# Optimization experiments

Hardware: AMD Instinct MI355X
Metric: run time of the kernel (lower is better)

Reference implementation:

```python
import jax, jax.numpy as jnp
import numpy as np

D_MODEL = 1024
H = 16
T = 1024
B = 8

def setup_inputs() -> dict:
    key = jax.random.key(0)
    k0, k1, k2, k3, k4 = jax.random.split(key, 5)
    return {
        "x": jax.random.normal(k0, (B, T, D_MODEL), dtype=jnp.float32),
        "Wq": jax.random.normal(k1, (D_MODEL, D_MODEL), dtype=jnp.float32),
        "Wk": jax.random.normal(k2, (D_MODEL, D_MODEL), dtype=jnp.float32),
        "Wv": jax.random.normal(k3, (D_MODEL, D_MODEL), dtype=jnp.float32),
        "Wp": jax.random.normal(k4, (D_MODEL, D_MODEL), dtype=jnp.float32),
    }

def reference(x, Wq, Wk, Wv, Wp):
    b, t, d = x.shape
    dh = d // H
    # projections
    q = (x @ Wq).reshape(b, t, H, dh)
    k = (x @ Wk).reshape(b, t, H, dh)
    v = (x @ Wv).reshape(b, t, H, dh)
    # [b, h, t, t] attention scores, scaled by sqrt(d_head)
    scores = jnp.einsum("bqhd,bkhd->bhqk", q, k) / jnp.sqrt(jnp.float32(dh))
    attn = jax.nn.softmax(scores, axis=-1)
    # [b, h, t, dh] -> [b, t, d]
    out = jnp.einsum("bhqk,bkhd->bqhd", attn, v).reshape(b, t, d)
    return out @ Wp
```

## Files before the change

kernel.cpp:

```cpp
#include <hip/hip_runtime.h>
#include <math.h>


typedef unsigned short u16;
typedef unsigned int u32;
typedef __bf16  bf16x8 __attribute__((ext_vector_type(8)));
typedef unsigned short u16x8 __attribute__((ext_vector_type(8)));
typedef unsigned short u16x4 __attribute__((ext_vector_type(4)));
typedef short s16x4 __attribute__((ext_vector_type(4)));
typedef unsigned int u32x2 __attribute__((ext_vector_type(2)));
typedef float f32x4 __attribute__((ext_vector_type(4)));

#define MFMA16(a,b,c) __builtin_amdgcn_mfma_f32_16x16x32_bf16((a),(b),(c),0,0,0)
#define MFMA16K16(a,b,c) __builtin_amdgcn_mfma_f32_16x16x16bf16_1k((a),(b),(c),0,0,0)

static __device__ __forceinline__ u16 f2b(float f){
  unsigned u = __builtin_bit_cast(unsigned, f);
  u += 0x7fffu + ((u >> 16) & 1u);
  return (u16)(u >> 16);
}
static __device__ __forceinline__ float b2f(u16 h){
  unsigned u = ((unsigned)h) << 16;
  return __builtin_bit_cast(float, u);
}
static __device__ __forceinline__ bf16x8 ldsfrag(const u16* p){
  return __builtin_bit_cast(bf16x8, *(const u16x8*)p);
}
static __device__ __forceinline__ u32 packhi(float fa, float fb){
  return __builtin_amdgcn_perm(__builtin_bit_cast(u32, fa),
                               __builtin_bit_cast(u32, fb), 0x07060302u);
}
static __device__ __forceinline__ void gld16(const void* g, void* l){
  __builtin_amdgcn_global_load_lds(
      (const __attribute__((address_space(1))) void*)g,
      (__attribute__((address_space(3))) void*)l, 16, 0, 0);
}


__global__ __launch_bounds__(256) void split_x_kernel(
    const float* __restrict__ x, u16* __restrict__ xh, u16* __restrict__ xl, int n)
{
  int i = (blockIdx.x * 256 + threadIdx.x) * 8;
  if (i >= n) return;
  float4 v0 = *(const float4*)(x + i);
  float4 v1 = *(const float4*)(x + i + 4);
  float vv[8] = {v0.x, v0.y, v0.z, v0.w, v1.x, v1.y, v1.z, v1.w};
  u16x8 hv, lv;
#pragma unroll
  for (int j = 0; j < 8; j++){
    u16 hb = f2b(vv[j]);
    hv[j] = hb;
    lv[j] = f2b(vv[j] - b2f(hb));
  }
  *(u16x8*)(xh + i) = hv;
  *(u16x8*)(xl + i) = lv;
}

__global__ __launch_bounds__(256) void transpose4_kernel(
    const float* __restrict__ Wq, const float* __restrict__ Wk,
    const float* __restrict__ Wv, const float* __restrict__ Wp,
    u16* __restrict__ qh_, u16* __restrict__ ql_,
    u16* __restrict__ kh_, u16* __restrict__ kl_,
    u16* __restrict__ vt_, u16* __restrict__ pt_)
{
  __shared__ float t[32][33];
  const int z = blockIdx.z;
  const float* W = (z == 0) ? Wq : (z == 1) ? Wk : (z == 2) ? Wv : Wp;
  u16* Th = (z == 0) ? qh_ : (z == 1) ? kh_ : (z == 2) ? vt_ : pt_;
  u16* Tl = (z == 0) ? ql_ : (z == 1) ? kl_ : nullptr;
  int n0 = blockIdx.x * 32, k0 = blockIdx.y * 32;
  int tx = threadIdx.x, ty = threadIdx.y;
#pragma unroll
  for (int i = 0; i < 4; i++){
    int k = k0 + ty + i * 8;
    t[ty + i * 8][tx] = W[(size_t)k * 1024 + n0 + tx];
  }
  __syncthreads();
#pragma unroll
  for (int i = 0; i < 4; i++){
    int n = n0 + ty + i * 8;
    float v = t[tx][ty + i * 8];
    u16 h = f2b(v);
    Th[(size_t)n * 1024 + k0 + tx] = h;
    if (Tl) Tl[(size_t)n * 1024 + k0 + tx] = f2b(v - b2f(h));
  }
}

template<int OUTMODE>
__global__ __launch_bounds__(256) void gemm_bt_kernel(
    const u16* __restrict__ A, const u16* __restrict__ Bt, void* __restrict__ Cv,
    int M, int N, int K)
{
  __shared__ __attribute__((aligned(16))) u16 lA[4096], lB[4096];
  const int tid = threadIdx.x, lane = tid & 63, wave = tid >> 6;
  const int quad = lane >> 4, l15 = lane & 15;
  const int row0 = blockIdx.x * 128, col0 = blockIdx.y * 128;
  const int wm = wave >> 1, wn = wave & 1;
  const int sr = lane >> 2, sc = (lane & 3) * 8;
  f32x4 acc[4][4];
#pragma unroll
  for (int mt = 0; mt < 4; mt++)
#pragma unroll
    for (int nt = 0; nt < 4; nt++) acc[mt][nt] = (f32x4)0.0f;

  for (int k0 = 0; k0 < K; k0 += 32){
#pragma unroll
    for (int i = 0; i < 2; i++){
      int c = wave * 2 + i;
      gld16(A  + (size_t)(row0 + c * 16 + sr) * K + k0 + sc, &lA[c * 512]);
      gld16(Bt + (size_t)(col0 + c * 16 + sr) * K + k0 + sc, &lB[c * 512]);
    }
    __syncthreads();
    bf16x8 a[4], b[4];
#pragma unroll
    for (int t = 0; t < 4; t++){
      a[t] = ldsfrag(&lA[(wm * 64 + t * 16 + l15) * 32 + quad * 8]);
      b[t] = ldsfrag(&lB[(wn * 64 + t * 16 + l15) * 32 + quad * 8]);
    }
#pragma unroll
    for (int mt = 0; mt < 4; mt++)
#pragma unroll
      for (int nt = 0; nt < 4; nt++)
        acc[mt][nt] = MFMA16(a[mt], b[nt], acc[mt][nt]);
    __syncthreads();
  }
  if (OUTMODE == 2){
#pragma unroll
    for (int mt = 0; mt < 4; mt++)
#pragma unroll
      for (int nt = 0; nt < 4; nt++){
        int row = row0 + wm * 64 + mt * 16 + quad * 4;
        int col = col0 + wn * 64 + nt * 16 + l15;
        int bb = row >> 10, tt = row & 1023;
        int hh = (col >> 6) & 15, d = col & 63;
        int bhI = bb * 16 + hh;
        int ktile = tt >> 7, fkt = (tt >> 4) & 7, qF = (tt >> 2) & 3;
        int nd = d >> 4, l15F = d & 15;
        size_t idx = ((((size_t)(bhI * 8 + ktile) * 8 + fkt) * 4 + nd) * 64
                      + qF * 16 + l15F) * 4;
        u16x4 vals;
#pragma unroll
        for (int r = 0; r < 4; r++) vals[r] = f2b(acc[mt][nt][r]);
        *(u16x4*)(((u16*)Cv) + idx) = vals;
      }
  } else {
#pragma unroll
    for (int mt = 0; mt < 4; mt++)
#pragma unroll
      for (int nt = 0; nt < 4; nt++)
#pragma unroll
        for (int r = 0; r < 4; r++){
          int row = row0 + wm * 64 + mt * 16 + quad * 4 + r;
          int col = col0 + wn * 64 + nt * 16 + l15;
          ((float*)Cv)[(size_t)row * N + col] = acc[mt][nt][r];
        }
  }
}

__global__ __launch_bounds__(512, 2) void gemm_qk_kernel(
    const u16* __restrict__ Ah, const u16* __restrict__ Al,
    const u16* __restrict__ Bh, const u16* __restrict__ Bl,
    u16* __restrict__ Qhf, u16* __restrict__ Qlf,
    u16* __restrict__ Khf, u16* __restrict__ Klf, int M, int N, int K)
{
  __shared__ __attribute__((aligned(16))) u16 sA[2][2][8192], sB[2][2][8192];
  const int tid = threadIdx.x, lane = tid & 63, wave = tid >> 6;
  const int quad = lane >> 4, l15 = lane & 15;
  const int wm = wave >> 2, wn = wave & 3;
  const int row0 = blockIdx.x * 256, col0 = blockIdx.y * 256;
  const int f0a = (wave & 3) | ((wave & 4) << 1);
  const int f0b = (wave & 1) | ((wave >> 1) << 2);
  const size_t fstride = (size_t)16 * K;
  const size_t abase = (size_t)(row0 + l15) * K + quad * 8;
  const size_t bbase = (size_t)(col0 + l15) * K + quad * 8;
  (void)M; (void)N;

  f32x4 acc[8][4];
#pragma unroll
  for (int mt = 0; mt < 8; mt++)
#pragma unroll
    for (int nt = 0; nt < 4; nt++) acc[mt][nt] = (f32x4)0.0f;

#define STAGE_G0(KK, NB) do {                                              \
    gld16(Ah + abase + (size_t)f0a * fstride + (KK), &sA[NB][0][f0a * 512]); \
    gld16(Al + abase + (size_t)f0a * fstride + (KK), &sA[NB][1][f0a * 512]); \
    gld16(Bh + bbase + (size_t)f0b * fstride + (KK), &sB[NB][0][f0b * 512]); \
    gld16(Bl + bbase + (size_t)f0b * fstride + (KK), &sB[NB][1][f0b * 512]); \
  } while (0)
#define STAGE_G1(KK, NB) do {                                                        \
    gld16(Bh + bbase + (size_t)(f0b + 2) * fstride + (KK), &sB[NB][0][(f0b + 2) * 512]); \
    gld16(Bl + bbase + (size_t)(f0b + 2) * fstride + (KK), &sB[NB][1][(f0b + 2) * 512]); \
  } while (0)
#define STAGE_G2(KK, NB) do {                                                        \
    gld16(Ah + abase + (size_t)(f0a + 4) * fstride + (KK), &sA[NB][0][(f0a + 4) * 512]); \
    gld16(Al + abase + (size_t)(f0a + 4) * fstride + (KK), &sA[NB][1][(f0a + 4) * 512]); \
  } while (0)
#define RD_A(B4, BUF) do {                                        \
    _Pragma("unroll")                                             \
    for (int i = 0; i < 4; i++){                                  \
      int fa = wm * 8 + (B4) + i;                                 \
      ahf[i] = ldsfrag(&sA[BUF][0][fa * 512 + lane * 8]);         \
      alf[i] = ldsfrag(&sA[BUF][1][fa * 512 + lane * 8]);         \
    } } while (0)
#define RD_B(B2, BUF) do {                                        \
    _Pragma("unroll")                                             \
    for (int j = 0; j < 2; j++){                                  \
      int fb = wn * 4 + (B2) + j;                                 \
      bhf[j] = ldsfrag(&sB[BUF][0][fb * 512 + lane * 8]);         \
      blf[j] = ldsfrag(&sB[BUF][1][fb * 512 + lane * 8]);         \
    } } while (0)
#define MM(M0, N0) do {                                                      \
    __builtin_amdgcn_s_setprio(1);                                           \
    _Pragma("unroll")                                                        \
    for (int i = 0; i < 4; i++)                                              \
      _Pragma("unroll")                                                      \
      for (int j = 0; j < 2; j++){                                           \
        acc[(M0) + i][(N0) + j] = MFMA16(alf[i], bhf[j], acc[(M0) + i][(N0) + j]); \
        acc[(M0) + i][(N0) + j] = MFMA16(ahf[i], blf[j], acc[(M0) + i][(N0) + j]); \
        acc[(M0) + i][(N0) + j] = MFMA16(ahf[i], bhf[j], acc[(M0) + i][(N0) + j]); \
      }                                                                      \
    __builtin_amdgcn_s_setprio(0);                                           \
  } while (0)
#define VMCNT4() asm volatile("s_waitcnt vmcnt(4)" ::: "memory")
#define VMCNT6() asm volatile("s_waitcnt vmcnt(6)" ::: "memory")
#define BARRIER() asm volatile("s_barrier" ::: "memory")

  const int NT = K >> 5;
  STAGE_G0(0, 0);
  STAGE_G1(0, 0);
  STAGE_G2(0, 0);

  bf16x8 ahf[4], alf[4], bhf[2], blf[2];
#pragma unroll 2
  for (int t = 0; t < NT; t++){
    const int buf = t & 1, nb = buf ^ 1;
    const int kn = ((t + 1) & (NT - 1)) * 32;
    VMCNT4();
    BARRIER();
    RD_A(0, buf);
    RD_B(0, buf);
    STAGE_G0(kn, nb);
    MM(0, 0);
    VMCNT6();
    BARRIER();
    RD_B(2, buf);
    STAGE_G1(kn, nb);
    MM(0, 2);
    VMCNT6();
    BARRIER();
    RD_A(4, buf);
    STAGE_G2(kn, nb);
    MM(4, 2);
    RD_B(0, buf);
    MM(4, 0);
  }
  asm volatile("s_waitcnt vmcnt(0)" ::: "memory");

#undef STAGE_G0
#undef STAGE_G1
#undef STAGE_G2
#undef RD_A
#undef RD_B
#undef MM
#undef VMCNT4
#undef VMCNT6
#undef BARRIER

  const bool isQ = (col0 < 1024);
#pragma unroll
  for (int mt = 0; mt < 8; mt++)
#pragma unroll
    for (int nt = 0; nt < 4; nt++)
#pragma unroll
      for (int r = 0; r < 4; r++){
        int row = row0 + wm * 128 + mt * 16 + quad * 4 + r;
        int col = col0 + wn * 64 + nt * 16 + l15;
        int bb = row >> 10, tt = row & 1023;
        int hh = (col >> 6) & 15, d = col & 63;
        int bhI = bb * 16 + hh;
        int kc = d >> 5, qF = (d >> 3) & 3, j = d & 7;
        float v = acc[mt][nt][r];
        u16 hi = f2b(v);
        u16 lo = f2b(v - b2f(hi));
        if (isQ){
          int qtile = tt >> 7, rr = tt & 127;
          int wv = rr >> 5, mtF = (rr >> 4) & 1, l15F = tt & 15;
          size_t idx = ((((size_t)(bhI * 8 + qtile) * 4 + wv) * 2 + mtF) * 2 + kc) * 512
                       + (qF * 16 + l15F) * 8 + j;
          Qhf[idx] = hi; Qlf[idx] = lo;
        } else {
          int ktile = tt >> 7, fkt = (tt >> 4) & 7, l15F = tt & 15;
          size_t idx = (((size_t)(bhI * 8 + ktile) * 8 + fkt) * 2 + kc) * 512
                       + (qF * 16 + l15F) * 8 + j;
          Khf[idx] = hi; Klf[idx] = lo;
        }
      }
}

__global__ __launch_bounds__(256, 3) void attn_kernel(
    const u16* __restrict__ Qhf, const u16* __restrict__ Qlf,
    const u16* __restrict__ Khf, const u16* __restrict__ Klf,
    const u16* __restrict__ Vf, u16* __restrict__ O)
{
  __shared__ __attribute__((aligned(16))) u16 lKh[2][4096], lKl[2][4096], lV[2][4096];
  const int tid = threadIdx.x, lane = tid & 63, wave = tid >> 6;
  const int quad = lane >> 4, l15 = lane & 15;
  const int qt = blockIdx.x >> 7, bh = blockIdx.x & 127;
  const int b = bh >> 4, h = bh & 15;
  const int q0 = qt * 128;
  const float BETA = 0.18033688011112042f;

  bf16x8 qh[2][2], ql[2][2];
  {
    size_t qbase = (size_t)(bh * 8 + qt) * 8192 + wave * 2048 + lane * 8;
    u16* sh = &lKh[0][0];  u16* sl = &lKl[0][0];
#pragma unroll
    for (int i = 0; i < 4; i++){
      gld16(Qhf + qbase + i * 512, sh + wave * 2048 + i * 512);
      gld16(Qlf + qbase + i * 512, sl + wave * 2048 + i * 512);
    }
    __syncthreads();
#pragma unroll
    for (int mt = 0; mt < 2; mt++)
#pragma unroll
      for (int kc = 0; kc < 2; kc++){
        int off = wave * 2048 + (mt * 2 + kc) * 512 + lane * 8;
        qh[mt][kc] = ldsfrag(sh + off);
        ql[mt][kc] = ldsfrag(sl + off);
      }
    __syncthreads();
  }

  float m_i[2] = {-3.0e38f, -3.0e38f}, l_i[2] = {0.0f, 0.0f};
  f32x4 o_acc[2][4];
#pragma unroll
  for (int mt = 0; mt < 2; mt++)
#pragma unroll
    for (int nd = 0; nd < 4; nd++) o_acc[mt][nd] = (f32x4)0.0f;

  const size_t pan = (size_t)bh * 65536;
#pragma unroll
  for (int i = 0; i < 2; i++){
    int c = wave * 2 + i;
    gld16(Khf + pan + c * 512 + lane * 8, &lKh[0][c * 512]);
    gld16(Klf + pan + c * 512 + lane * 8, &lKl[0][c * 512]);
    gld16(Vf  + pan + c * 512 + lane * 8, &lV [0][c * 512]);
  }

#pragma unroll 1
  for (int j = 0; j < 16; j++){
    const int cur = j & 1;
    __syncthreads();
    if (j < 15){
      size_t nb = pan + (size_t)(j + 1) * 4096;
      const int nxt = cur ^ 1;
#pragma unroll
      for (int i = 0; i < 2; i++){
        int c = wave * 2 + i;
        gld16(Khf + nb + c * 512 + lane * 8, &lKh[nxt][c * 512]);
        gld16(Klf + nb + c * 512 + lane * 8, &lKl[nxt][c * 512]);
        gld16(Vf  + nb + c * 512 + lane * 8, &lV [nxt][c * 512]);
      }
    }

    f32x4 s[2][4];
#pragma unroll
    for (int qt2 = 0; qt2 < 2; qt2++)
#pragma unroll
      for (int f4 = 0; f4 < 4; f4++) s[qt2][f4] = (f32x4)0.0f;
#pragma unroll
    for (int f4 = 0; f4 < 4; f4++){
      int aoff = f4 * 1024 + lane * 8;
      bf16x8 kh0 = ldsfrag(&lKh[cur][aoff]);
      bf16x8 kh1 = ldsfrag(&lKh[cur][aoff + 512]);
      bf16x8 kl0 = ldsfrag(&lKl[cur][aoff]);
      bf16x8 kl1 = ldsfrag(&lKl[cur][aoff + 512]);
      __builtin_amdgcn_s_setprio(1);
#pragma unroll
      for (int qt2 = 0; qt2 < 2; qt2++){
        s[qt2][f4] = MFMA16(kl0, qh[qt2][0], s[qt2][f4]);
        s[qt2][f4] = MFMA16(kl1, qh[qt2][1], s[qt2][f4]);
        s[qt2][f4] = MFMA16(kh0, ql[qt2][0], s[qt2][f4]);
        s[qt2][f4] = MFMA16(kh1, ql[qt2][1], s[qt2][f4]);
        s[qt2][f4] = MFMA16(kh0, qh[qt2][0], s[qt2][f4]);
        s[qt2][f4] = MFMA16(kh1, qh[qt2][1], s[qt2][f4]);
      }
      __builtin_amdgcn_s_setprio(0);
    }

    float alpha[2];
#pragma unroll
    for (int qt2 = 0; qt2 < 2; qt2++){
      f32x4 mv = s[qt2][0];
#pragma unroll
      for (int f4 = 1; f4 < 4; f4++){
        mv[0] = fmaxf(mv[0], s[qt2][f4][0]); mv[1] = fmaxf(mv[1], s[qt2][f4][1]);
        mv[2] = fmaxf(mv[2], s[qt2][f4][2]); mv[3] = fmaxf(mv[3], s[qt2][f4][3]);
      }
      float mx = fmaxf(fmaxf(mv[0], mv[1]), fmaxf(mv[2], mv[3]));
      mx = fmaxf(mx, __shfl_xor(mx, 16));
      mx = fmaxf(mx, __shfl_xor(mx, 32));
      float mn = fmaxf(m_i[qt2], mx);
      alpha[qt2] = __builtin_amdgcn_exp2f((m_i[qt2] - mn) * BETA);
      m_i[qt2] = mn;
      float mb = mn * BETA;
      f32x4 ps = (f32x4)0.0f;
#pragma unroll
      for (int f4 = 0; f4 < 4; f4++)
#pragma unroll
        for (int r = 0; r < 4; r++){
          float p = __builtin_amdgcn_exp2f(s[qt2][f4][r] * BETA - mb);
          s[qt2][f4][r] = p;
          ps[r] += p;
        }
      float rs = (ps[0] + ps[1]) + (ps[2] + ps[3]);
      rs += __shfl_xor(rs, 16);
      rs += __shfl_xor(rs, 32);
      l_i[qt2] = l_i[qt2] * alpha[qt2] + rs;
    }

#pragma unroll
    for (int mt = 0; mt < 2; mt++)
#pragma unroll
      for (int r = 0; r < 4; r++){
        float ar = __shfl(alpha[mt], quad * 4 + r);
#pragma unroll
        for (int nd = 0; nd < 4; nd++) o_acc[mt][nd][r] *= ar;
      }

#pragma unroll
    for (int f4 = 0; f4 < 4; f4++){
      s16x4 vb[4];
#pragma unroll
      for (int nd = 0; nd < 4; nd++)
        vb[nd] = __builtin_bit_cast(s16x4,
                   *(const u16x4*)&lV[cur][(f4 * 4 + nd) * 256 + lane * 4]);
      __builtin_amdgcn_s_setprio(1);
#pragma unroll
      for (int qt2 = 0; qt2 < 2; qt2++){
        u32x2 pd;
        pd[0] = packhi(s[qt2][f4][1], s[qt2][f4][0]);
        pd[1] = packhi(s[qt2][f4][3], s[qt2][f4][2]);
        s16x4 pa = __builtin_bit_cast(s16x4, pd);
#pragma unroll
        for (int nd = 0; nd < 4; nd++)
          o_acc[qt2][nd] = MFMA16K16(pa, vb[nd], o_acc[qt2][nd]);
      }
      __builtin_amdgcn_s_setprio(0);
    }
  }

#pragma unroll
  for (int mt = 0; mt < 2; mt++)
#pragma unroll
    for (int r = 0; r < 4; r++){
      float lr = __shfl(l_i[mt], quad * 4 + r);
      float inv = 1.0f / lr;
      int t = q0 + wave * 32 + mt * 16 + quad * 4 + r;
      size_t rowoff = (size_t)(b * 1024 + t) * 1024 + h * 64;
#pragma unroll
      for (int nd = 0; nd < 4; nd++)
        O[rowoff + nd * 16 + l15] = f2b(o_acc[mt][nd][r] * inv);
    }
}

extern "C" void kernel_launch(void* const* d_in, const int* in_sizes, int n_in,
                              void* d_out, int out_size, void* d_ws, size_t ws_size,
                              hipStream_t stream)
{
  const float* x  = (const float*)d_in[0];
  const float* Wq = (const float*)d_in[1];
  const float* Wk = (const float*)d_in[2];
  const float* Wv = (const float*)d_in[3];
  const float* Wp = (const float*)d_in[4];
  float* out = (float*)d_out;
  char* ws = (char*)d_ws;
  const size_t MB = 1024 * 1024;
  u16* xh   = (u16*)(ws + 0);
  u16* xl   = (u16*)(ws + 16 * MB);
  u16* wqkh = (u16*)(ws + 32 * MB);
  u16* wqkl = (u16*)(ws + 36 * MB);
  u16* wvt  = (u16*)(ws + 40 * MB);
  u16* wpt  = (u16*)(ws + 42 * MB);
  u16* Qhf  = (u16*)(ws + 44 * MB);
  u16* Qlf  = (u16*)(ws + 60 * MB);
  u16* Khf  = (u16*)(ws + 76 * MB);
  u16* Klf  = (u16*)(ws + 92 * MB);
  u16* Vf   = (u16*)(ws + 108 * MB);
  u16* obuf = xh;
  (void)in_sizes; (void)n_in; (void)out_size; (void)ws_size;

  split_x_kernel<<<4096, 256, 0, stream>>>(x, xh, xl, 8 * 1024 * 1024);
  transpose4_kernel<<<dim3(32, 32, 4), dim3(32, 8), 0, stream>>>(
      Wq, Wk, Wv, Wp, wqkh, wqkl, wqkh + 1024 * 1024, wqkl + 1024 * 1024, wvt, wpt);
  gemm_qk_kernel<<<dim3(32, 8), 512, 0, stream>>>(xh, xl, wqkh, wqkl,
                                                  Qhf, Qlf, Khf, Klf, 8192, 2048, 1024);
  gemm_bt_kernel<2><<<dim3(64, 8), 256, 0, stream>>>(xh, wvt, (void*)Vf, 8192, 1024, 1024);
  attn_kernel<<<1024, 256, 0, stream>>>(Qhf, Qlf, Khf, Klf, Vf, obuf);
  gemm_bt_kernel<0><<<dim3(64, 8), 256, 0, stream>>>(obuf, wpt, (void*)out, 8192, 1024, 1024);
}
```

Baseline: 335.0 us.

## Double-buffer LDS tiles in bf16 GEMM with one barrier per k-step

```diff
diff --git a/kernel.cpp b/kernel.cpp
--- a/kernel.cpp
+++ b/kernel.cpp
@@ -91,39 +91,54 @@
     const u16* __restrict__ A, const u16* __restrict__ Bt, void* __restrict__ Cv,
     int M, int N, int K)
 {
-  __shared__ __attribute__((aligned(16))) u16 lA[4096], lB[4096];
+  __shared__ __attribute__((aligned(16))) u16 lA[2][4096], lB[2][4096];
   const int tid = threadIdx.x, lane = tid & 63, wave = tid >> 6;
   const int quad = lane >> 4, l15 = lane & 15;
   const int row0 = blockIdx.x * 128, col0 = blockIdx.y * 128;
   const int wm = wave >> 1, wn = wave & 1;
-  const int sr = lane >> 2, sc = (lane & 3) * 8;
+  const int c0 = wave * 2, c1 = wave * 2 + 1;
+  const size_t ar0 = (size_t)(row0 + c0 * 16 + l15) * K + quad * 8;
+  const size_t ar1 = (size_t)(row0 + c1 * 16 + l15) * K + quad * 8;
+  const size_t br0 = (size_t)(col0 + c0 * 16 + l15) * K + quad * 8;
+  const size_t br1 = (size_t)(col0 + c1 * 16 + l15) * K + quad * 8;
   f32x4 acc[4][4];
 #pragma unroll
   for (int mt = 0; mt < 4; mt++)
 #pragma unroll
     for (int nt = 0; nt < 4; nt++) acc[mt][nt] = (f32x4)0.0f;
 
-  for (int k0 = 0; k0 < K; k0 += 32){
-#pragma unroll
-    for (int i = 0; i < 2; i++){
-      int c = wave * 2 + i;
-      gld16(A  + (size_t)(row0 + c * 16 + sr) * K + k0 + sc, &lA[c * 512]);
-      gld16(Bt + (size_t)(col0 + c * 16 + sr) * K + k0 + sc, &lB[c * 512]);
-    }
-    __syncthreads();
+  const int NT = K >> 5;
+  gld16(A  + ar0, &lA[0][c0 * 512]);
+  gld16(A  + ar1, &lA[0][c1 * 512]);
+  gld16(Bt + br0, &lB[0][c0 * 512]);
+  gld16(Bt + br1, &lB[0][c1 * 512]);
+
+#pragma unroll 2
+  for (int t = 0; t < NT; t++){
+    const int buf = t & 1, nb = buf ^ 1;
+    const int kn = ((t + 1) & (NT - 1)) * 32;
+    asm volatile("s_waitcnt vmcnt(0)" ::: "memory");
+    asm volatile("s_barrier" ::: "memory");
+    gld16(A  + ar0 + kn, &lA[nb][c0 * 512]);
+    gld16(A  + ar1 + kn, &lA[nb][c1 * 512]);
+    gld16(Bt + br0 + kn, &lB[nb][c0 * 512]);
+    gld16(Bt + br1 + kn, &lB[nb][c1 * 512]);
     bf16x8 a[4], b[4];
 #pragma unroll
-    for (int t = 0; t < 4; t++){
-      a[t] = ldsfrag(&lA[(wm * 64 + t * 16 + l15) * 32 + quad * 8]);
-      b[t] = ldsfrag(&lB[(wn * 64 + t * 16 + l15) * 32 + quad * 8]);
-    }
+    for (int f = 0; f < 4; f++){
+      a[f] = ldsfrag(&lA[buf][(wm * 4 + f) * 512 + lane * 8]);
+      b[f] = ldsfrag(&lB[buf][(wn * 4 + f) * 512 + lane * 8]);
+    }
+    __builtin_amdgcn_s_setprio(1);
 #pragma unroll
     for (int mt = 0; mt < 4; mt++)
 #pragma unroll
       for (int nt = 0; nt < 4; nt++)
         acc[mt][nt] = MFMA16(a[mt], b[nt], acc[mt][nt]);
-    __syncthreads();
-  }
+    __builtin_amdgcn_s_setprio(0);
+  }
+  asm volatile("s_waitcnt vmcnt(0)" ::: "memory");
+
   if (OUTMODE == 2){
 #pragma unroll
     for (int mt = 0; mt < 4; mt++)
```

After: 356.0 us. 6.3% more time.

## Process two query tiles per attention block to reuse K/V panels

Applied to the files above, without the earlier changes.

```diff
diff --git a/kernel.cpp b/kernel.cpp
--- a/kernel.cpp
+++ b/kernel.cpp
@@ -297,7 +297,7 @@
       }
 }
 
-__global__ __launch_bounds__(256, 3) void attn_kernel(
+__global__ __launch_bounds__(256, 2) void attn_kernel(
     const u16* __restrict__ Qhf, const u16* __restrict__ Qlf,
     const u16* __restrict__ Khf, const u16* __restrict__ Klf,
     const u16* __restrict__ Vf, u16* __restrict__ O)
@@ -307,36 +307,42 @@
   const int quad = lane >> 4, l15 = lane & 15;
   const int qt = blockIdx.x >> 7, bh = blockIdx.x & 127;
   const int b = bh >> 4, h = bh & 15;
-  const int q0 = qt * 128;
+  const int q0 = qt * 256;
   const float BETA = 0.18033688011112042f;
 
-  bf16x8 qh[2][2], ql[2][2];
+  bf16x8 qh[2][2][2], ql[2][2][2];
   {
-    size_t qbase = (size_t)(bh * 8 + qt) * 8192 + wave * 2048 + lane * 8;
     u16* sh = &lKh[0][0];  u16* sl = &lKl[0][0];
 #pragma unroll
-    for (int i = 0; i < 4; i++){
-      gld16(Qhf + qbase + i * 512, sh + wave * 2048 + i * 512);
-      gld16(Qlf + qbase + i * 512, sl + wave * 2048 + i * 512);
+    for (int g = 0; g < 2; g++){
+      size_t qbase = ((size_t)((bh * 8 + 2 * qt + g) * 4 + wave)) * 2048 + lane * 8;
+#pragma unroll
+      for (int i = 0; i < 4; i++){
+        gld16(Qhf + qbase + i * 512, sh + wave * 2048 + i * 512);
+        gld16(Qlf + qbase + i * 512, sl + wave * 2048 + i * 512);
+      }
+      __syncthreads();
+#pragma unroll
+      for (int mt = 0; mt < 2; mt++)
+#pragma unroll
+        for (int kc = 0; kc < 2; kc++){
+          int off = wave * 2048 + (mt * 2 + kc) * 512 + lane * 8;
+          qh[g][mt][kc] = ldsfrag(sh + off);
+          ql[g][mt][kc] = ldsfrag(sl + off);
+        }
+      __syncthreads();
     }
-    __syncthreads();
+  }
+
+  float m_i[2][2] = {{-3.0e38f, -3.0e38f}, {-3.0e38f, -3.0e38f}};
+  float l_i[2][2] = {{0.0f, 0.0f}, {0.0f, 0.0f}};
+  f32x4 o_acc[2][2][4];
+#pragma unroll
+  for (int g = 0; g < 2; g++)
 #pragma unroll
     for (int mt = 0; mt < 2; mt++)
 #pragma unroll
-      for (int kc = 0; kc < 2; kc++){
-        int off = wave * 2048 + (mt * 2 + kc) * 512 + lane * 8;
-        qh[mt][kc] = ldsfrag(sh + off);
-        ql[mt][kc] = ldsfrag(sl + off);
-      }
-    __syncthreads();
-  }
-
-  float m_i[2] = {-3.0e38f, -3.0e38f}, l_i[2] = {0.0f, 0.0f};
-  f32x4 o_acc[2][4];
-#pragma unroll
-  for (int mt = 0; mt < 2; mt++)
-#pragma unroll
-    for (int nd = 0; nd < 4; nd++) o_acc[mt][nd] = (f32x4)0.0f;
+      for (int nd = 0; nd < 4; nd++) o_acc[g][mt][nd] = (f32x4)0.0f;
 
   const size_t pan = (size_t)bh * 65536;
 #pragma unroll
@@ -363,105 +369,110 @@
       }
     }
 
-    f32x4 s[2][4];
-#pragma unroll
-    for (int qt2 = 0; qt2 < 2; qt2++)
-#pragma unroll
-      for (int f4 = 0; f4 < 4; f4++) s[qt2][f4] = (f32x4)0.0f;
-#pragma unroll
-    for (int f4 = 0; f4 < 4; f4++){
-      int aoff = f4 * 1024 + lane * 8;
-      bf16x8 kh0 = ldsfrag(&lKh[cur][aoff]);
-      bf16x8 kh1 = ldsfrag(&lKh[cur][aoff + 512]);
-      bf16x8 kl0 = ldsfrag(&lKl[cur][aoff]);
-      bf16x8 kl1 = ldsfrag(&lKl[cur][aoff + 512]);
-      __builtin_amdgcn_s_setprio(1);
+#pragma unroll
+    for (int g = 0; g < 2; g++){
+      f32x4 s[2][4];
+#pragma unroll
+      for (int qt2 = 0; qt2 < 2; qt2++)
+#pragma unroll
+        for (int f4 = 0; f4 < 4; f4++) s[qt2][f4] = (f32x4)0.0f;
+#pragma unroll
+      for (int f4 = 0; f4 < 4; f4++){
+        int aoff = f4 * 1024 + lane * 8;
+        bf16x8 kh0 = ldsfrag(&lKh[cur][aoff]);
+        bf16x8 kh1 = ldsfrag(&lKh[cur][aoff + 512]);
+        bf16x8 kl0 = ldsfrag(&lKl[cur][aoff]);
+        bf16x8 kl1 = ldsfrag(&lKl[cur][aoff + 512]);
+        __builtin_amdgcn_s_setprio(1);
+#pragma unroll
+        for (int qt2 = 0; qt2 < 2; qt2++){
+          s[qt2][f4] = MFMA16(kl0, qh[g][qt2][0], s[qt2][f4]);
+          s[qt2][f4] = MFMA16(kl1, qh[g][qt2][1], s[qt2][f4]);
+          s[qt2][f4] = MFMA16(kh0, ql[g][qt2][0], s[qt2][f4]);
+          s[qt2][f4] = MFMA16(kh1, ql[g][qt2][1], s[qt2][f4]);
+          s[qt2][f4] = MFMA16(kh0, qh[g][qt2][0], s[qt2][f4]);
+          s[qt2][f4] = MFMA16(kh1, qh[g][qt2][1], s[qt2][f4]);
+        }
+        __builtin_amdgcn_s_setprio(0);
+      }
+
+      float alpha[2];
 #pragma unroll
       for (int qt2 = 0; qt2 < 2; qt2++){
-        s[qt2][f4] = MFMA16(kl0, qh[qt2][0], s[qt2][f4]);
-        s[qt2][f4] = MFMA16(kl1, qh[qt2][1], s[qt2][f4]);
-        s[qt2][f4] = MFMA16(kh0, ql[qt2][0], s[qt2][f4]);
-        s[qt2][f4] = MFMA16(kh1, ql[qt2][1], s[qt2][f4]);
-        s[qt2][f4] = MFMA16(kh0, qh[qt2][0], s[qt2][f4]);
-        s[qt2][f4] = MFMA16(kh1, qh[qt2][1], s[qt2][f4]);
-      }
-      __builtin_amdgcn_s_setprio(0);
+        f32x4 mv = s[qt2][0];
+#pragma unroll
+        for (int f4 = 1; f4 < 4; f4++){
+          mv[0] = fmaxf(mv[0], s[qt2][f4][0]); mv[1] = fmaxf(mv[1], s[qt2][f4][1]);
+          mv[2] = fmaxf(mv[2], s[qt2][f4][2]); mv[3] = fmaxf(mv[3], s[qt2][f4][3]);
+        }
+        float mx = fmaxf(fmaxf(mv[0], mv[1]), fmaxf(mv[2], mv[3]));
+        mx = fmaxf(mx, __shfl_xor(mx, 16));
+        mx = fmaxf(mx, __shfl_xor(mx, 32));
+        float mn = fmaxf(m_i[g][qt2], mx);
+        alpha[qt2] = __builtin_amdgcn_exp2f((m_i[g][qt2] - mn) * BETA);
+        m_i[g][qt2] = mn;
+        float mb = mn * BETA;
+        f32x4 ps = (f32x4)0.0f;
+#pragma unroll
+        for (int f4 = 0; f4 < 4; f4++)
+#pragma unroll
+          for (int r = 0; r < 4; r++){
+            float p = __builtin_amdgcn_exp2f(s[qt2][f4][r] * BETA - mb);
+            s[qt2][f4][r] = p;
+            ps[r] += p;
+          }
+        float rs = (ps[0] + ps[1]) + (ps[2] + ps[3]);
+        rs += __shfl_xor(rs, 16);
+        rs += __shfl_xor(rs, 32);
+        l_i[g][qt2] = l_i[g][qt2] * alpha[qt2] + rs;
+      }
+
+#pragma unroll
+      for (int mt = 0; mt < 2; mt++)
+#pragma unroll
+        for (int r = 0; r < 4; r++){
+          float ar = __shfl(alpha[mt], quad * 4 + r);
+#pragma unroll
+          for (int nd = 0; nd < 4; nd++) o_acc[g][mt][nd][r] *= ar;
+        }
+
+#pragma unroll
+      for (int f4 = 0; f4 < 4; f4++){
+        s16x4 vb[4];
+#pragma unroll
+        for (int nd = 0; nd < 4; nd++)
+          vb[nd] = __builtin_bit_cast(s16x4,
+                     *(const u16x4*)&lV[cur][(f4 * 4 + nd) * 256 + lane * 4]);
+        __builtin_amdgcn_s_setprio(1);
+#pragma unroll
+        for (int qt2 = 0; qt2 < 2; qt2++){
+          u32x2 pd;
+          pd[0] = packhi(s[qt2][f4][1], s[qt2][f4][0]);
+          pd[1] = packhi(s[qt2][f4][3], s[qt2][f4][2]);
+          s16x4 pa = __builtin_bit_cast(s16x4, pd);
+#pragma unroll
+          for (int nd = 0; nd < 4; nd++)
+            o_acc[g][qt2][nd] = MFMA16K16(pa, vb[nd], o_acc[g][qt2][nd]);
+        }
+        __builtin_amdgcn_s_setprio(0);
+      }
     }
-
-    float alpha[2];
-#pragma unroll
-    for (int qt2 = 0; qt2 < 2; qt2++){
-      f32x4 mv = s[qt2][0];
-#pragma unroll
-      for (int f4 = 1; f4 < 4; f4++){
-        mv[0] = fmaxf(mv[0], s[qt2][f4][0]); mv[1] = fmaxf(mv[1], s[qt2][f4][1]);
-        mv[2] = fmaxf(mv[2], s[qt2][f4][2]); mv[3] = fmaxf(mv[3], s[qt2][f4][3]);
-      }
-      float mx = fmaxf(fmaxf(mv[0], mv[1]), fmaxf(mv[2], mv[3]));
-      mx = fmaxf(mx, __shfl_xor(mx, 16));
-      mx = fmaxf(mx, __shfl_xor(mx, 32));
-      float mn = fmaxf(m_i[qt2], mx);
-      alpha[qt2] = __builtin_amdgcn_exp2f((m_i[qt2] - mn) * BETA);
-      m_i[qt2] = mn;
-      float mb = mn * BETA;
-      f32x4 ps = (f32x4)0.0f;
-#pragma unroll
-      for (int f4 = 0; f4 < 4; f4++)
-#pragma unroll
-        for (int r = 0; r < 4; r++){
-          float p = __builtin_amdgcn_exp2f(s[qt2][f4][r] * BETA - mb);
-          s[qt2][f4][r] = p;
-          ps[r] += p;
-        }
-      float rs = (ps[0] + ps[1]) + (ps[2] + ps[3]);
-      rs += __shfl_xor(rs, 16);
-      rs += __shfl_xor(rs, 32);
-      l_i[qt2] = l_i[qt2] * alpha[qt2] + rs;
-    }
-
+  }
+
+#pragma unroll
+  for (int g = 0; g < 2; g++)
 #pragma unroll
     for (int mt = 0; mt < 2; mt++)
 #pragma unroll
       for (int r = 0; r < 4; r++){
-        float ar = __shfl(alpha[mt], quad * 4 + r);
-#pragma unroll
-        for (int nd = 0; nd < 4; nd++) o_acc[mt][nd][r] *= ar;
-      }
-
-#pragma unroll
-    for (int f4 = 0; f4 < 4; f4++){
-      s16x4 vb[4];
-#pragma unroll
-      for (int nd = 0; nd < 4; nd++)
-        vb[nd] = __builtin_bit_cast(s16x4,
-                   *(const u16x4*)&lV[cur][(f4 * 4 + nd) * 256 + lane * 4]);
-      __builtin_amdgcn_s_setprio(1);
-#pragma unroll
-      for (int qt2 = 0; qt2 < 2; qt2++){
-        u32x2 pd;
-        pd[0] = packhi(s[qt2][f4][1], s[qt2][f4][0]);
-        pd[1] = packhi(s[qt2][f4][3], s[qt2][f4][2]);
-        s16x4 pa = __builtin_bit_cast(s16x4, pd);
+        float lr = __shfl(l_i[g][mt], quad * 4 + r);
+        float inv = 1.0f / lr;
+        int t = q0 + g * 128 + wave * 32 + mt * 16 + quad * 4 + r;
+        size_t rowoff = (size_t)(b * 1024 + t) * 1024 + h * 64;
 #pragma unroll
         for (int nd = 0; nd < 4; nd++)
-          o_acc[qt2][nd] = MFMA16K16(pa, vb[nd], o_acc[qt2][nd]);
-      }
-      __builtin_amdgcn_s_setprio(0);
-    }
-  }
-
-#pragma unroll
-  for (int mt = 0; mt < 2; mt++)
-#pragma unroll
-    for (int r = 0; r < 4; r++){
-      float lr = __shfl(l_i[mt], quad * 4 + r);
-      float inv = 1.0f / lr;
-      int t = q0 + wave * 32 + mt * 16 + quad * 4 + r;
-      size_t rowoff = (size_t)(b * 1024 + t) * 1024 + h * 64;
-#pragma unroll
-      for (int nd = 0; nd < 4; nd++)
-        O[rowoff + nd * 16 + l15] = f2b(o_acc[mt][nd][r] * inv);
-    }
+          O[rowoff + nd * 16 + l15] = f2b(o_acc[g][mt][nd][r] * inv);
+      }
 }
 
 extern "C" void kernel_launch(void* const* d_in, const int* in_sizes, int n_in,
@@ -496,6 +507,6 @@
   gemm_qk_kernel<<<dim3(32, 8), 512, 0, stream>>>(xh, xl, wqkh, wqkl,
                                                   Qhf, Qlf, Khf, Klf, 8192, 2048, 1024);
   gemm_bt_kernel<2><<<dim3(64, 8), 256, 0, stream>>>(xh, wvt, (void*)Vf, 8192, 1024, 1024);
-  attn_kernel<<<1024, 256, 0, stream>>>(Qhf, Qlf, Khf, Klf, Vf, obuf);
+  attn_kernel<<<512, 256, 0, stream>>>(Qhf, Qlf, Khf, Klf, Vf, obuf);
   gemm_bt_kernel<0><<<dim3(64, 8), 256, 0, stream>>>(obuf, wpt, (void*)out, 8192, 1024, 1024);
 }
```

Measured after the change: 334.8 us. No clear change (-0.1%).
